# Kernel tuning notes

Hardware: AMD Instinct MI355X
Metric: run time of the kernel (lower is better)

Reference implementation:

```python
import jax, jax.numpy as jnp
import numpy as np

B, S, D, F, O = 4, 2048, 1024, 4096, 1024
E, NS, K = 4, 2, 2  # routed experts, shared experts, topk


def setup_inputs() -> dict:
    key = jax.random.key(0)
    ks = jax.random.split(key, 6)
    def w(k, shape, fan_in):
        return jax.random.normal(k, shape, jnp.float32) * (fan_in ** -0.5)
    return {
        "x": jax.random.normal(ks[0], (B, S, D), jnp.float32),
        "gate_w": w(ks[1], (D, E), D),
        "gate_b": jnp.zeros((E,), jnp.float32),
        "sw1": w(ks[2], (NS, D, F), D),  # shared experts, first linear
        "sb1": jnp.zeros((NS, F), jnp.float32),
        "sw2": w(ks[3], (NS, F, O), F),
        "sb2": jnp.zeros((NS, O), jnp.float32),
        "rw1": w(ks[4], (E, D, F), D),   # routed experts, first linear
        "rb1": jnp.zeros((E, F), jnp.float32),
        "rw2": w(ks[5], (E, F, O), F),
        "rb2": jnp.zeros((E, O), jnp.float32),
    }


def reference(x, gate_w, gate_b, sw1, sb1, sw2, sb2, rw1, rb1, rw2, rb2):
    # Gating (eval mode: no noise)
    weights = jax.nn.softmax(x @ gate_w + gate_b, axis=-1)      # [B,S,E]
    topk_w, topk_i = jax.lax.top_k(weights, K)                  # [B,S,K]

    # Shared experts: average of NS expert MLPs
    sh = jax.nn.relu(jnp.einsum('bsd,ndf->bsnf', x, sw1) + sb1)
    shared = (jnp.einsum('bsnf,nfo->bsno', sh, sw2) + sb2).sum(axis=2) / NS  # [B,S,O]

    # Routed experts: every expert applied densely, then one-hot-select topk.
    # Original computes expert(expanded_x) where expanded_x repeats x K times;
    # the result is identical per copy, so compute once per expert and gather.
    rh = jax.nn.relu(jnp.einsum('bsd,edf->bsef', x, rw1) + rb1)  # [B,S,E,F]
    eo = jnp.einsum('bsef,efo->bseo', rh, rw2) + rb2             # [B,S,E,O]
    gathered = jnp.take_along_axis(eo, topk_i[..., None], axis=2)  # [B,S,K,O]
    routed = (gathered * topk_w[..., None]).sum(axis=2)          # [B,S,O]

    return shared + routed
```

## Files before the change

kernel.cpp:

```cpp
#include <hip/hip_runtime.h>

typedef __bf16 bf16_t;
typedef __bf16 bf16x8 __attribute__((ext_vector_type(8)));
typedef float f32x4 __attribute__((ext_vector_type(4)));

constexpr int Tn = 4 * 2048;
constexpr int Dd = 1024;
constexpr int Ff = 4096;
constexpr int Oo = 1024;
constexpr int NEXP = 6;

__device__ __forceinline__ float ldin(const void* p, size_t i, int isf32) {
    return isf32 ? ((const float*)p)[i] : (float)((const bf16_t*)p)[i];
}

__global__ void detect_kernel(const unsigned int* __restrict__ xw, int* __restrict__ flag) {
    __shared__ int cnt;
    if (threadIdx.x == 0) cnt = 0;
    __syncthreads();
    int c = 0;
    for (int i = threadIdx.x; i < 16384; i += 256) {
        unsigned w = xw[i];
        if (((w >> 7) & 0xFFu) == 0xFFu) ++c;
    }
    atomicAdd(&cnt, c);
    __syncthreads();
    if (threadIdx.x == 0) flag[0] = (cnt >= 4) ? 1 : 0;
}

__global__ void cvt_x_kernel(const void* __restrict__ x, const int* __restrict__ flag,
                             bf16_t* __restrict__ xb) {
    int f = flag[0];
    size_t i = (size_t)blockIdx.x * 256 + threadIdx.x;
    xb[i] = (bf16_t)ldin(x, i, f);
}

__global__ void cvt_transpose_kernel(const void* __restrict__ src, size_t eofs,
                                     const int* __restrict__ flag,
                                     bf16_t* __restrict__ dst, int R, int C) {
    __shared__ bf16_t tile[32][33];
    int f = flag[0];
    int c0 = blockIdx.x * 32, r0 = blockIdx.y * 32;
    int tx = threadIdx.x, ty = threadIdx.y;
    #pragma unroll
    for (int i = 0; i < 32; i += 8)
        tile[ty + i][tx] = (bf16_t)ldin(src, eofs + (size_t)(r0 + ty + i) * C + c0 + tx, f);
    __syncthreads();
    #pragma unroll
    for (int i = 0; i < 32; i += 8)
        dst[(size_t)(c0 + ty + i) * R + r0 + tx] = tile[tx][ty + i];
}

__global__ void gate_kernel(const void* __restrict__ x, const void* __restrict__ gw,
                            const void* __restrict__ gb, const int* __restrict__ flag,
                            float* __restrict__ coef) {
    int f = flag[0];
    int t = blockIdx.x;
    int lane = threadIdx.x;
    float a0 = 0.f, a1 = 0.f, a2 = 0.f, a3 = 0.f;
    for (int d = lane; d < Dd; d += 64) {
        float xv = ldin(x, (size_t)t * Dd + d, f);
        a0 += xv * ldin(gw, (size_t)d * 4 + 0, f);
        a1 += xv * ldin(gw, (size_t)d * 4 + 1, f);
        a2 += xv * ldin(gw, (size_t)d * 4 + 2, f);
        a3 += xv * ldin(gw, (size_t)d * 4 + 3, f);
    }
    #pragma unroll
    for (int off = 32; off; off >>= 1) {
        a0 += __shfl_xor(a0, off);
        a1 += __shfl_xor(a1, off);
        a2 += __shfl_xor(a2, off);
        a3 += __shfl_xor(a3, off);
    }
    if (lane == 0) {
        float l[4] = {a0 + ldin(gb, 0, f), a1 + ldin(gb, 1, f),
                      a2 + ldin(gb, 2, f), a3 + ldin(gb, 3, f)};
        float mx = fmaxf(fmaxf(l[0], l[1]), fmaxf(l[2], l[3]));
        float e[4], s = 0.f;
        #pragma unroll
        for (int i = 0; i < 4; ++i) { e[i] = expf(l[i] - mx); s += e[i]; }
        float w[4];
        #pragma unroll
        for (int i = 0; i < 4; ++i) w[i] = e[i] / s;
        int i0 = 0;
        for (int i = 1; i < 4; ++i) if (w[i] > w[i0]) i0 = i;
        int i1 = -1;
        for (int i = 0; i < 4; ++i) { if (i == i0) continue; if (i1 < 0 || w[i] > w[i1]) i1 = i; }
        float c[8] = {0.5f, 0.5f, 0.f, 0.f, 0.f, 0.f, 0.f, 0.f};
        c[2 + i0] = w[i0];
        c[2 + i1] = w[i1];
        float* dst = coef + (size_t)t * 8;
        #pragma unroll
        for (int k = 0; k < 8; ++k) dst[k] = c[k];
    }
}

__global__ void init_acc_kernel(const float* __restrict__ coef, const void* __restrict__ sb2,
                                const void* __restrict__ rb2, const int* __restrict__ flag,
                                float* __restrict__ acc) {
    int f = flag[0];
    size_t idx = (size_t)blockIdx.x * 256 + threadIdx.x;
    int t = (int)(idx >> 10);
    int o = (int)(idx & 1023);
    const float* c = coef + (size_t)t * 8;
    float v = c[0] * ldin(sb2, o, f) + c[1] * ldin(sb2, Oo + o, f)
            + c[2] * ldin(rb2, o, f) + c[3] * ldin(rb2, Oo + o, f)
            + c[4] * ldin(rb2, 2 * Oo + o, f) + c[5] * ldin(rb2, 3 * Oo + o, f);
    acc[idx] = v;
}

__global__ void convert_kernel(const float* __restrict__ acc, const int* __restrict__ flag,
                               void* __restrict__ out) {
    int f = flag[0];
    size_t idx = (size_t)blockIdx.x * 256 + threadIdx.x;
    float v = acc[idx];
    if (v != v) v = 333.0f;
    if (f) ((float*)out)[idx] = v;
    else   ((bf16_t*)out)[idx] = (bf16_t)v;
}

template <int MODE>
__launch_bounds__(256, 2)
__global__ void gemm_kernel(const bf16_t* __restrict__ A, const bf16_t* __restrict__ Bt,
                            int M, int N, int K,
                            const void* __restrict__ bias, size_t b1_e,
                            const int* __restrict__ flag,
                            const float* __restrict__ coef,
                            bf16_t* __restrict__ obf, float* __restrict__ oacc) {
    constexpr int BM = 128, BN = 128, BK = 64;
    __shared__ __align__(16) bf16_t Al[BM * BK];
    __shared__ __align__(16) bf16_t Bl[BN * BK];

    const int tid = threadIdx.x;
    const int lane = tid & 63;
    const int wave = tid >> 6;
    const int wm = wave & 1, wn = wave >> 1;
    const int bm = blockIdx.x * BM;
    const int bn = blockIdx.y * BN;
    const int l15 = lane & 15;
    const int l4 = lane >> 4;
    const int r7 = l15 & 7;

    f32x4 acc[4][4] = {};

    for (int k0 = 0; k0 < K; k0 += BK) {
        #pragma unroll
        for (int it = 0; it < 4; ++it) {
            int q = it * 256 + tid;
            int row = q >> 3, c8s = q & 7;
            int k8 = c8s ^ (row & 7);
            const bf16_t* g = A + (size_t)(bm + row) * K + k0 + k8 * 8;
            __builtin_amdgcn_global_load_lds(
                (const __attribute__((address_space(1))) unsigned int*)g,
                (__attribute__((address_space(3))) unsigned int*)(&Al[q * 8]), 16, 0, 0);
        }
        #pragma unroll
        for (int it = 0; it < 4; ++it) {
            int q = it * 256 + tid;
            int row = q >> 3, c8s = q & 7;
            int k8 = c8s ^ (row & 7);
            const bf16_t* g = Bt + (size_t)(bn + row) * K + k0 + k8 * 8;
            __builtin_amdgcn_global_load_lds(
                (const __attribute__((address_space(1))) unsigned int*)g,
                (__attribute__((address_space(3))) unsigned int*)(&Bl[q * 8]), 16, 0, 0);
        }
        __syncthreads();
        #pragma unroll
        for (int kk = 0; kk < BK; kk += 32) {
            const int k8f = l4 + (kk >> 3);
            const int c8s = (k8f ^ r7) * 8;
            bf16x8 af[4], bfv[4];
            #pragma unroll
            for (int i = 0; i < 4; ++i)
                af[i] = *(const bf16x8*)&Al[(wm * 64 + i * 16 + l15) * BK + c8s];
            #pragma unroll
            for (int j = 0; j < 4; ++j)
                bfv[j] = *(const bf16x8*)&Bl[(wn * 64 + j * 16 + l15) * BK + c8s];
            #pragma unroll
            for (int i = 0; i < 4; ++i)
                #pragma unroll
                for (int j = 0; j < 4; ++j)
                    acc[i][j] = __builtin_amdgcn_mfma_f32_16x16x32_bf16(af[i], bfv[j], acc[i][j], 0, 0, 0);
        }
        __syncthreads();
    }

    if (MODE == 1) {
        int isf32 = flag[0];
        float bz[4];
        #pragma unroll
        for (int j = 0; j < 4; ++j)
            bz[j] = ldin(bias, b1_e + (size_t)(bn + wn * 64 + j * 16 + l15), isf32);
        #pragma unroll
        for (int i = 0; i < 4; ++i) {
            #pragma unroll
            for (int r = 0; r < 4; ++r) {
                int m = bm + wm * 64 + i * 16 + l4 * 4 + r;
                float cf = coef[(size_t)m * 8];
                #pragma unroll
                for (int j = 0; j < 4; ++j) {
                    float v = acc[i][j][r] + bz[j];
                    v = fmaxf(v, 0.f) * cf;
                    obf[(size_t)m * N + bn + wn * 64 + j * 16 + l15] = (bf16_t)v;
                }
            }
        }
    } else {
        #pragma unroll
        for (int i = 0; i < 4; ++i) {
            #pragma unroll
            for (int r = 0; r < 4; ++r) {
                int m = bm + wm * 64 + i * 16 + l4 * 4 + r;
                float* orow = oacc + (size_t)m * N + bn + wn * 64 + l15;
                #pragma unroll
                for (int j = 0; j < 4; ++j)
                    orow[j * 16] += acc[i][j][r];
            }
        }
    }
}

extern "C" void kernel_launch(void* const* d_in, const int* in_sizes, int n_in,
                              void* d_out, int out_size, void* d_ws, size_t ws_size,
                              hipStream_t stream) {
    const void* x      = d_in[0];
    const void* gate_w = d_in[1];
    const void* gate_b = d_in[2];
    const void* sw1    = d_in[3];
    const void* sb1    = d_in[4];
    const void* sw2    = d_in[5];
    const void* sb2    = d_in[6];
    const void* rw1    = d_in[7];
    const void* rb1    = d_in[8];
    const void* rw2    = d_in[9];
    const void* rb2    = d_in[10];

    char* ws = (char*)d_ws;
    int* flag = (int*)ws;
    size_t off = 256;
    bf16_t* W1T = (bf16_t*)(ws + off); off += (size_t)Ff * Dd * sizeof(bf16_t);
    bf16_t* W2T = (bf16_t*)(ws + off); off += (size_t)Oo * Ff * sizeof(bf16_t);
    bf16_t* xb  = (bf16_t*)(ws + off); off += (size_t)Tn * Dd * sizeof(bf16_t);
    float* coef = (float*)(ws + off);  off += (size_t)Tn * 8 * sizeof(float);
    float* accb = (float*)(ws + off);  off += (size_t)Tn * Oo * sizeof(float);
    bf16_t* Hs  = (bf16_t*)(ws + off);
    size_t rem = (ws_size > off) ? (ws_size - off) : 0;
    long tcap = (long)(rem / ((size_t)Ff * sizeof(bf16_t)));
    int Tc = (int)((tcap / 128) * 128);
    if (Tc < 128) Tc = 128;
    if (Tc > Tn) Tc = Tn;

    detect_kernel<<<1, 256, 0, stream>>>((const unsigned int*)x, flag);
    cvt_x_kernel<<<(Tn * Dd) / 256, 256, 0, stream>>>(x, flag, xb);
    gate_kernel<<<Tn, 64, 0, stream>>>(x, gate_w, gate_b, flag, coef);
    init_acc_kernel<<<(Tn * Oo) / 256, 256, 0, stream>>>(coef, sb2, rb2, flag, accb);

    dim3 tb(32, 8);
    for (int j = 0; j < NEXP; ++j) {
        const void* w1 = (j < 2) ? sw1 : rw1;
        const void* w2 = (j < 2) ? sw2 : rw2;
        const void* b1 = (j < 2) ? sb1 : rb1;
        int je = (j < 2) ? j : (j - 2);
        size_t w1_e = (size_t)je * Dd * Ff;
        size_t w2_e = (size_t)je * Ff * Oo;
        size_t b1_e = (size_t)je * Ff;

        cvt_transpose_kernel<<<dim3(Ff / 32, Dd / 32), tb, 0, stream>>>(w1, w1_e, flag, W1T, Dd, Ff);
        cvt_transpose_kernel<<<dim3(Oo / 32, Ff / 32), tb, 0, stream>>>(w2, w2_e, flag, W2T, Ff, Oo);

        for (int tok0 = 0; tok0 < Tn; tok0 += Tc) {
            int tc = (Tn - tok0 < Tc) ? (Tn - tok0) : Tc;
            gemm_kernel<1><<<dim3(tc / 128, Ff / 128), 256, 0, stream>>>(
                xb + (size_t)tok0 * Dd, W1T, tc, Ff, Dd,
                b1, b1_e, flag, coef + (size_t)tok0 * 8 + j, Hs, nullptr);
            gemm_kernel<2><<<dim3(tc / 128, Oo / 128), 256, 0, stream>>>(
                Hs, W2T, tc, Oo, Ff, nullptr, 0, flag, nullptr, nullptr, accb + (size_t)tok0 * Oo);
        }
    }

    convert_kernel<<<(Tn * Oo) / 256, 256, 0, stream>>>(accb, flag, d_out);
}
```

Measured before the change: 1.211 ms.

## Double-buffer GEMM LDS tiles with 256-row blocks, 8 waves and XCD-aware block remap

Reworks the bf16 MFMA GEMM to use 256x256 (first linear) and 256x128 (second linear) tiles with 512 threads. LDS is double-buffered so global-to-LDS loads for step t+2 overlap the MFMAs of step t, with hand-placed waitcnt and barriers. It also adds s_setprio around MFMA bursts and remaps block IDs so that blocks sharing tiles are grouped, aiming at better L2 locality across the XCDs. Larger tiles raise arithmetic intensity but increase register and LDS pressure, and they reduce the number of blocks available to fill the CUs.

Measured after the change: 1.402 ms. 15.8% more time.

```diff
diff --git a/kernel.cpp b/kernel.cpp
--- a/kernel.cpp
+++ b/kernel.cpp
@@ -119,101 +119,169 @@
     else   ((bf16_t*)out)[idx] = (bf16_t)v;
 }
 
-template <int MODE>
-__launch_bounds__(256, 2)
+template <int MODE, int BN_, int WM_>
+__launch_bounds__(512, 2)
 __global__ void gemm_kernel(const bf16_t* __restrict__ A, const bf16_t* __restrict__ Bt,
                             int M, int N, int K,
                             const void* __restrict__ bias, size_t b1_e,
                             const int* __restrict__ flag,
                             const float* __restrict__ coef,
                             bf16_t* __restrict__ obf, float* __restrict__ oacc) {
-    constexpr int BM = 128, BN = 128, BK = 64;
-    __shared__ __align__(16) bf16_t Al[BM * BK];
-    __shared__ __align__(16) bf16_t Bl[BN * BK];
+    constexpr int BM = 256, BK = 64;
+    constexpr int WN_ = 8 / WM_;
+    constexpr int NI = 16 / WM_;
+    constexpr int NJ = BN_ / (WN_ * 16);
+    constexpr int NIH = NI / 2;
+    constexpr int NJH = NJ / 2;
+    constexpr int ALOADS = 4;
+    constexpr int BLOADS = BN_ / 64;
+    constexpr int TOT = ALOADS + BLOADS;
+
+    __shared__ __align__(16) bf16_t Al[2][BM * BK];
+    __shared__ __align__(16) bf16_t Bl[2][BN_ * BK];
 
     const int tid = threadIdx.x;
     const int lane = tid & 63;
     const int wave = tid >> 6;
-    const int wm = wave & 1, wn = wave >> 1;
-    const int bm = blockIdx.x * BM;
-    const int bn = blockIdx.y * BN;
+    const int wm = wave / WN_;
+    const int wn = wave % WN_;
     const int l15 = lane & 15;
     const int l4 = lane >> 4;
     const int r7 = l15 & 7;
 
-    f32x4 acc[4][4] = {};
-
-    for (int k0 = 0; k0 < K; k0 += BK) {
-        #pragma unroll
-        for (int it = 0; it < 4; ++it) {
-            int q = it * 256 + tid;
-            int row = q >> 3, c8s = q & 7;
-            int k8 = c8s ^ (row & 7);
+    const int gx = gridDim.x;
+    const int nwg = gx * gridDim.y;
+    const int id = blockIdx.y * gx + blockIdx.x;
+    const int cpx = nwg >> 3;
+    const int sid = (id & 7) * cpx + (id >> 3);
+    const int bm = (sid % gx) * BM;
+    const int bn = (sid / gx) * BN_;
+
+    const int nK = K / BK;
+
+    auto stage = [&](int t, int b) {
+        const int k0 = t * BK;
+        #pragma unroll
+        for (int it = 0; it < ALOADS; ++it) {
+            int q = it * 512 + tid;
+            int row = q >> 3, c8 = q & 7;
+            int k8 = c8 ^ (row & 7);
             const bf16_t* g = A + (size_t)(bm + row) * K + k0 + k8 * 8;
             __builtin_amdgcn_global_load_lds(
                 (const __attribute__((address_space(1))) unsigned int*)g,
-                (__attribute__((address_space(3))) unsigned int*)(&Al[q * 8]), 16, 0, 0);
-        }
-        #pragma unroll
-        for (int it = 0; it < 4; ++it) {
-            int q = it * 256 + tid;
-            int row = q >> 3, c8s = q & 7;
-            int k8 = c8s ^ (row & 7);
+                (__attribute__((address_space(3))) unsigned int*)(&Al[b][q * 8]), 16, 0, 0);
+        }
+        #pragma unroll
+        for (int it = 0; it < BLOADS; ++it) {
+            int q = it * 512 + tid;
+            int row = q >> 3, c8 = q & 7;
+            int k8 = c8 ^ (row & 7);
             const bf16_t* g = Bt + (size_t)(bn + row) * K + k0 + k8 * 8;
             __builtin_amdgcn_global_load_lds(
                 (const __attribute__((address_space(1))) unsigned int*)g,
-                (__attribute__((address_space(3))) unsigned int*)(&Bl[q * 8]), 16, 0, 0);
-        }
-        __syncthreads();
-        #pragma unroll
-        for (int kk = 0; kk < BK; kk += 32) {
-            const int k8f = l4 + (kk >> 3);
-            const int c8s = (k8f ^ r7) * 8;
-            bf16x8 af[4], bfv[4];
+                (__attribute__((address_space(3))) unsigned int*)(&Bl[b][q * 8]), 16, 0, 0);
+        }
+    };
+
+    f32x4 acc[NI][NJ] = {};
+
+    stage(0, 0);
+    if (nK > 1) {
+        stage(1, 1);
+        if constexpr (TOT == 8) asm volatile("s_waitcnt vmcnt(8)" ::: "memory");
+        else                    asm volatile("s_waitcnt vmcnt(6)" ::: "memory");
+    } else {
+        asm volatile("s_waitcnt vmcnt(0)" ::: "memory");
+    }
+    __builtin_amdgcn_sched_barrier(0);
+    __builtin_amdgcn_s_barrier();
+    __builtin_amdgcn_sched_barrier(0);
+
+    const int a_off0 = ((l4 + 0) ^ r7) * 8;
+    const int a_off1 = ((l4 + 4) ^ r7) * 8;
+    const int arow = wm * (NI * 16) + l15;
+    const int brow = wn * (NJ * 16) + l15;
+
+    for (int t = 0; t < nK; ++t) {
+        const bf16_t* __restrict__ Ab = Al[t & 1];
+        const bf16_t* __restrict__ Bb = Bl[t & 1];
+        bf16x8 bfv[NJ][2];
+        bf16x8 af[NIH][2];
+        #pragma unroll
+        for (int j = 0; j < NJ; ++j) {
+            bfv[j][0] = *(const bf16x8*)&Bb[(brow + j * 16) * BK + a_off0];
+            bfv[j][1] = *(const bf16x8*)&Bb[(brow + j * 16) * BK + a_off1];
+        }
+        #pragma unroll
+        for (int ih = 0; ih < 2; ++ih) {
             #pragma unroll
-            for (int i = 0; i < 4; ++i)
-                af[i] = *(const bf16x8*)&Al[(wm * 64 + i * 16 + l15) * BK + c8s];
+            for (int i = 0; i < NIH; ++i) {
+                af[i][0] = *(const bf16x8*)&Ab[(arow + (ih * NIH + i) * 16) * BK + a_off0];
+                af[i][1] = *(const bf16x8*)&Ab[(arow + (ih * NIH + i) * 16) * BK + a_off1];
+            }
             #pragma unroll
-            for (int j = 0; j < 4; ++j)
-                bfv[j] = *(const bf16x8*)&Bl[(wn * 64 + j * 16 + l15) * BK + c8s];
-            #pragma unroll
-            for (int i = 0; i < 4; ++i)
+            for (int jh = 0; jh < 2; ++jh) {
+                __builtin_amdgcn_s_setprio(1);
                 #pragma unroll
-                for (int j = 0; j < 4; ++j)
-                    acc[i][j] = __builtin_amdgcn_mfma_f32_16x16x32_bf16(af[i], bfv[j], acc[i][j], 0, 0, 0);
-        }
-        __syncthreads();
+                for (int kx = 0; kx < 2; ++kx)
+                    #pragma unroll
+                    for (int i = 0; i < NIH; ++i)
+                        #pragma unroll
+                        for (int j = 0; j < NJH; ++j)
+                            acc[ih * NIH + i][jh * NJH + j] =
+                                __builtin_amdgcn_mfma_f32_16x16x32_bf16(
+                                    af[i][kx], bfv[jh * NJH + j][kx],
+                                    acc[ih * NIH + i][jh * NJH + j], 0, 0, 0);
+                __builtin_amdgcn_s_setprio(0);
+            }
+        }
+        if (t + 1 < nK) {
+            asm volatile("s_waitcnt lgkmcnt(0)" ::: "memory");
+            __builtin_amdgcn_sched_barrier(0);
+            __builtin_amdgcn_s_barrier();
+            __builtin_amdgcn_sched_barrier(0);
+            if (t + 2 < nK) {
+                stage(t + 2, t & 1);
+                if constexpr (TOT == 8) asm volatile("s_waitcnt vmcnt(8)" ::: "memory");
+                else                    asm volatile("s_waitcnt vmcnt(6)" ::: "memory");
+            } else {
+                asm volatile("s_waitcnt vmcnt(0)" ::: "memory");
+            }
+            __builtin_amdgcn_sched_barrier(0);
+            __builtin_amdgcn_s_barrier();
+            __builtin_amdgcn_sched_barrier(0);
+        }
     }
 
     if (MODE == 1) {
-        int isf32 = flag[0];
-        float bz[4];
-        #pragma unroll
-        for (int j = 0; j < 4; ++j)
-            bz[j] = ldin(bias, b1_e + (size_t)(bn + wn * 64 + j * 16 + l15), isf32);
-        #pragma unroll
-        for (int i = 0; i < 4; ++i) {
+        const int isf32 = flag[0];
+        float bz[NJ];
+        #pragma unroll
+        for (int j = 0; j < NJ; ++j)
+            bz[j] = ldin(bias, b1_e + (size_t)(bn + wn * (NJ * 16) + j * 16 + l15), isf32);
+        #pragma unroll
+        for (int i = 0; i < NI; ++i) {
             #pragma unroll
             for (int r = 0; r < 4; ++r) {
-                int m = bm + wm * 64 + i * 16 + l4 * 4 + r;
+                int m = bm + wm * (NI * 16) + i * 16 + l4 * 4 + r;
                 float cf = coef[(size_t)m * 8];
                 #pragma unroll
-                for (int j = 0; j < 4; ++j) {
+                for (int j = 0; j < NJ; ++j) {
                     float v = acc[i][j][r] + bz[j];
                     v = fmaxf(v, 0.f) * cf;
-                    obf[(size_t)m * N + bn + wn * 64 + j * 16 + l15] = (bf16_t)v;
+                    obf[(size_t)m * N + bn + wn * (NJ * 16) + j * 16 + l15] = (bf16_t)v;
                 }
             }
         }
     } else {
         #pragma unroll
-        for (int i = 0; i < 4; ++i) {
+        for (int i = 0; i < NI; ++i) {
             #pragma unroll
             for (int r = 0; r < 4; ++r) {
-                int m = bm + wm * 64 + i * 16 + l4 * 4 + r;
-                float* orow = oacc + (size_t)m * N + bn + wn * 64 + l15;
+                int m = bm + wm * (NI * 16) + i * 16 + l4 * 4 + r;
+                float* orow = oacc + (size_t)m * N + bn + wn * (NJ * 16) + l15;
                 #pragma unroll
-                for (int j = 0; j < 4; ++j)
+                for (int j = 0; j < NJ; ++j)
                     orow[j * 16] += acc[i][j][r];
             }
         }
@@ -246,8 +314,8 @@
     bf16_t* Hs  = (bf16_t*)(ws + off);
     size_t rem = (ws_size > off) ? (ws_size - off) : 0;
     long tcap = (long)(rem / ((size_t)Ff * sizeof(bf16_t)));
-    int Tc = (int)((tcap / 128) * 128);
-    if (Tc < 128) Tc = 128;
+    int Tc = (int)((tcap / 256) * 256);
+    if (Tc < 256) Tc = 256;
     if (Tc > Tn) Tc = Tn;
 
     detect_kernel<<<1, 256, 0, stream>>>((const unsigned int*)x, flag);
@@ -270,11 +338,12 @@
 
         for (int tok0 = 0; tok0 < Tn; tok0 += Tc) {
             int tc = (Tn - tok0 < Tc) ? (Tn - tok0) : Tc;
-            gemm_kernel<1><<<dim3(tc / 128, Ff / 128), 256, 0, stream>>>(
+            gemm_kernel<1, 256, 2><<<dim3(tc / 256, Ff / 256), 512, 0, stream>>>(
                 xb + (size_t)tok0 * Dd, W1T, tc, Ff, Dd,
                 b1, b1_e, flag, coef + (size_t)tok0 * 8 + j, Hs, nullptr);
-            gemm_kernel<2><<<dim3(tc / 128, Oo / 128), 256, 0, stream>>>(
-                Hs, W2T, tc, Oo, Ff, nullptr, 0, flag, nullptr, nullptr, accb + (size_t)tok0 * Oo);
+            gemm_kernel<2, 128, 4><<<dim3(tc / 256, Oo / 128), 512, 0, stream>>>(
+                Hs, W2T, tc, Oo, Ff, nullptr, 0, flag, nullptr, nullptr,
+                accb + (size_t)tok0 * Oo);
         }
     }
 
```

## Gather routed tokens per expert and run routed GEMMs only on selected rows

Applied to the files above, without the earlier changes.

The gate kernel now builds a per-expert token list with atomics. A finalize kernel pads each list to 128 rows, pointing padded entries at a dummy token whose coefficient is zero. Routed-expert GEMMs gather A rows through that list and scatter-accumulate outputs by token index. Blocks beyond the expert's padded count exit early, so each routed expert processes only about half the tokens instead of all of them. In exchange this adds atomics, indirect loads and scattered stores, and the dummy row reads past the end of xb.

Result: slower. 1.303 ms (+7.6%).

```diff
diff --git a/kernel.cpp b/kernel.cpp
--- a/kernel.cpp
+++ b/kernel.cpp
@@ -8,7 +8,6 @@
 constexpr int Dd = 1024;
 constexpr int Ff = 4096;
 constexpr int Oo = 1024;
-constexpr int NEXP = 6;
 
 __device__ __forceinline__ float ldin(const void* p, size_t i, int isf32) {
     return isf32 ? ((const float*)p)[i] : (float)((const bf16_t*)p)[i];
@@ -26,6 +25,10 @@
     atomicAdd(&cnt, c);
     __syncthreads();
     if (threadIdx.x == 0) flag[0] = (cnt >= 4) ? 1 : 0;
+}
+
+__global__ void zero_cnt_kernel(int* __restrict__ cnt) {
+    if (threadIdx.x < 4) cnt[threadIdx.x] = 0;
 }
 
 __global__ void cvt_x_kernel(const void* __restrict__ x, const int* __restrict__ flag,
@@ -53,7 +56,8 @@
 
 __global__ void gate_kernel(const void* __restrict__ x, const void* __restrict__ gw,
                             const void* __restrict__ gb, const int* __restrict__ flag,
-                            float* __restrict__ coef) {
+                            float* __restrict__ coef, int* __restrict__ cnt,
+                            int* __restrict__ tlist) {
     int f = flag[0];
     int t = blockIdx.x;
     int lane = threadIdx.x;
@@ -92,7 +96,24 @@
         float* dst = coef + (size_t)t * 8;
         #pragma unroll
         for (int k = 0; k < 8; ++k) dst[k] = c[k];
-    }
+        int p0 = atomicAdd(&cnt[i0], 1);
+        tlist[(size_t)i0 * Tn + p0] = t;
+        int p1 = atomicAdd(&cnt[i1], 1);
+        tlist[(size_t)i1 * Tn + p1] = t;
+    }
+}
+
+__global__ void finalize_route_kernel(const int* __restrict__ cnt, int* __restrict__ cntp,
+                                      int* __restrict__ tlist, float* __restrict__ coef) {
+    int lane = threadIdx.x;
+    #pragma unroll
+    for (int e = 0; e < 4; ++e) {
+        int c = cnt[e]; if (c > Tn) c = Tn;
+        int p = (c + 127) & ~127;
+        if (lane == 0) cntp[e] = p;
+        for (int i = c + lane; i < p; i += 64) tlist[(size_t)e * Tn + i] = Tn;
+    }
+    if (lane < 8) coef[(size_t)Tn * 8 + lane] = 0.f;
 }
 
 __global__ void init_acc_kernel(const float* __restrict__ coef, const void* __restrict__ sb2,
@@ -126,8 +147,16 @@
                             const void* __restrict__ bias, size_t b1_e,
                             const int* __restrict__ flag,
                             const float* __restrict__ coef,
-                            bf16_t* __restrict__ obf, float* __restrict__ oacc) {
+                            bf16_t* __restrict__ obf, float* __restrict__ oacc,
+                            const int* __restrict__ tl, const int* __restrict__ cntp,
+                            int tok0, int joff) {
     constexpr int BM = 128, BN = 128, BK = 64;
+
+    if constexpr (MODE >= 3) {
+        int rem = cntp[0] - tok0;
+        if ((int)blockIdx.x * BM >= rem) return;
+    }
+
     __shared__ __align__(16) bf16_t Al[BM * BK];
     __shared__ __align__(16) bf16_t Bl[BN * BK];
 
@@ -141,6 +170,12 @@
     const int l4 = lane >> 4;
     const int r7 = l15 & 7;
 
+    int ar[4];
+    if constexpr (MODE == 3) {
+        #pragma unroll
+        for (int it = 0; it < 4; ++it) ar[it] = tl[bm + (tid >> 3) + it * 32];
+    }
+
     f32x4 acc[4][4] = {};
 
     for (int k0 = 0; k0 < K; k0 += BK) {
@@ -149,7 +184,11 @@
             int q = it * 256 + tid;
             int row = q >> 3, c8s = q & 7;
             int k8 = c8s ^ (row & 7);
-            const bf16_t* g = A + (size_t)(bm + row) * K + k0 + k8 * 8;
+            const bf16_t* g;
+            if constexpr (MODE == 3)
+                g = A + (size_t)ar[it] * K + k0 + k8 * 8;
+            else
+                g = A + (size_t)(bm + row) * K + k0 + k8 * 8;
             __builtin_amdgcn_global_load_lds(
                 (const __attribute__((address_space(1))) unsigned int*)g,
                 (__attribute__((address_space(3))) unsigned int*)(&Al[q * 8]), 16, 0, 0);
@@ -185,7 +224,7 @@
         __syncthreads();
     }
 
-    if (MODE == 1) {
+    if constexpr (MODE == 1 || MODE == 3) {
         int isf32 = flag[0];
         float bz[4];
         #pragma unroll
@@ -196,7 +235,13 @@
             #pragma unroll
             for (int r = 0; r < 4; ++r) {
                 int m = bm + wm * 64 + i * 16 + l4 * 4 + r;
-                float cf = coef[(size_t)m * 8];
+                float cf;
+                if constexpr (MODE == 3) {
+                    int token = tl[m];
+                    cf = coef[(size_t)token * 8 + joff];
+                } else {
+                    cf = coef[(size_t)m * 8];
+                }
                 #pragma unroll
                 for (int j = 0; j < 4; ++j) {
                     float v = acc[i][j][r] + bz[j];
@@ -211,7 +256,13 @@
             #pragma unroll
             for (int r = 0; r < 4; ++r) {
                 int m = bm + wm * 64 + i * 16 + l4 * 4 + r;
-                float* orow = oacc + (size_t)m * N + bn + wn * 64 + l15;
+                float* orow;
+                if constexpr (MODE == 4) {
+                    int token = tl[m];
+                    orow = oacc + (size_t)token * N + bn + wn * 64 + l15;
+                } else {
+                    orow = oacc + (size_t)m * N + bn + wn * 64 + l15;
+                }
                 #pragma unroll
                 for (int j = 0; j < 4; ++j)
                     orow[j * 16] += acc[i][j][r];
@@ -241,8 +292,14 @@
     bf16_t* W1T = (bf16_t*)(ws + off); off += (size_t)Ff * Dd * sizeof(bf16_t);
     bf16_t* W2T = (bf16_t*)(ws + off); off += (size_t)Oo * Ff * sizeof(bf16_t);
     bf16_t* xb  = (bf16_t*)(ws + off); off += (size_t)Tn * Dd * sizeof(bf16_t);
-    float* coef = (float*)(ws + off);  off += (size_t)Tn * 8 * sizeof(float);
-    float* accb = (float*)(ws + off);  off += (size_t)Tn * Oo * sizeof(float);
+    float* coef = (float*)(ws + off);  off += (size_t)(Tn + 1) * 8 * sizeof(float);
+    off = (off + 255) & ~(size_t)255;
+    int* cnt    = (int*)(ws + off);    off += 256;
+    int* cntp   = (int*)(ws + off);    off += 256;
+    int* tlist  = (int*)(ws + off);    off += (size_t)4 * Tn * sizeof(int);
+    off = (off + 255) & ~(size_t)255;
+    float* accb = (float*)(ws + off);  off += (size_t)(Tn + 1) * Oo * sizeof(float);
+    off = (off + 255) & ~(size_t)255;
     bf16_t* Hs  = (bf16_t*)(ws + off);
     size_t rem = (ws_size > off) ? (ws_size - off) : 0;
     long tcap = (long)(rem / ((size_t)Ff * sizeof(bf16_t)));
@@ -251,30 +308,47 @@
     if (Tc > Tn) Tc = Tn;
 
     detect_kernel<<<1, 256, 0, stream>>>((const unsigned int*)x, flag);
+    zero_cnt_kernel<<<1, 64, 0, stream>>>(cnt);
     cvt_x_kernel<<<(Tn * Dd) / 256, 256, 0, stream>>>(x, flag, xb);
-    gate_kernel<<<Tn, 64, 0, stream>>>(x, gate_w, gate_b, flag, coef);
+    gate_kernel<<<Tn, 64, 0, stream>>>(x, gate_w, gate_b, flag, coef, cnt, tlist);
+    finalize_route_kernel<<<1, 64, 0, stream>>>(cnt, cntp, tlist, coef);
     init_acc_kernel<<<(Tn * Oo) / 256, 256, 0, stream>>>(coef, sb2, rb2, flag, accb);
 
     dim3 tb(32, 8);
-    for (int j = 0; j < NEXP; ++j) {
-        const void* w1 = (j < 2) ? sw1 : rw1;
-        const void* w2 = (j < 2) ? sw2 : rw2;
-        const void* b1 = (j < 2) ? sb1 : rb1;
-        int je = (j < 2) ? j : (j - 2);
-        size_t w1_e = (size_t)je * Dd * Ff;
-        size_t w2_e = (size_t)je * Ff * Oo;
-        size_t b1_e = (size_t)je * Ff;
-
-        cvt_transpose_kernel<<<dim3(Ff / 32, Dd / 32), tb, 0, stream>>>(w1, w1_e, flag, W1T, Dd, Ff);
-        cvt_transpose_kernel<<<dim3(Oo / 32, Ff / 32), tb, 0, stream>>>(w2, w2_e, flag, W2T, Ff, Oo);
-
+
+    for (int j = 0; j < 2; ++j) {
+        size_t w1_e = (size_t)j * Dd * Ff;
+        size_t w2_e = (size_t)j * Ff * Oo;
+        size_t b1_e = (size_t)j * Ff;
+        cvt_transpose_kernel<<<dim3(Ff / 32, Dd / 32), tb, 0, stream>>>(sw1, w1_e, flag, W1T, Dd, Ff);
+        cvt_transpose_kernel<<<dim3(Oo / 32, Ff / 32), tb, 0, stream>>>(sw2, w2_e, flag, W2T, Ff, Oo);
         for (int tok0 = 0; tok0 < Tn; tok0 += Tc) {
             int tc = (Tn - tok0 < Tc) ? (Tn - tok0) : Tc;
             gemm_kernel<1><<<dim3(tc / 128, Ff / 128), 256, 0, stream>>>(
                 xb + (size_t)tok0 * Dd, W1T, tc, Ff, Dd,
-                b1, b1_e, flag, coef + (size_t)tok0 * 8 + j, Hs, nullptr);
+                sb1, b1_e, flag, coef + (size_t)tok0 * 8 + j, Hs, nullptr,
+                nullptr, nullptr, 0, 0);
             gemm_kernel<2><<<dim3(tc / 128, Oo / 128), 256, 0, stream>>>(
-                Hs, W2T, tc, Oo, Ff, nullptr, 0, flag, nullptr, nullptr, accb + (size_t)tok0 * Oo);
+                Hs, W2T, tc, Oo, Ff, nullptr, 0, flag, nullptr, nullptr,
+                accb + (size_t)tok0 * Oo, nullptr, nullptr, 0, 0);
+        }
+    }
+
+    for (int e = 0; e < 4; ++e) {
+        size_t w1_e = (size_t)e * Dd * Ff;
+        size_t w2_e = (size_t)e * Ff * Oo;
+        size_t b1_e = (size_t)e * Ff;
+        cvt_transpose_kernel<<<dim3(Ff / 32, Dd / 32), tb, 0, stream>>>(rw1, w1_e, flag, W1T, Dd, Ff);
+        cvt_transpose_kernel<<<dim3(Oo / 32, Ff / 32), tb, 0, stream>>>(rw2, w2_e, flag, W2T, Ff, Oo);
+        for (int tok0 = 0; tok0 < Tn; tok0 += Tc) {
+            int tc = (Tn - tok0 < Tc) ? (Tn - tok0) : Tc;
+            gemm_kernel<3><<<dim3(tc / 128, Ff / 128), 256, 0, stream>>>(
+                xb, W1T, tc, Ff, Dd,
+                rb1, b1_e, flag, coef, Hs, nullptr,
+                tlist + (size_t)e * Tn + tok0, cntp + e, tok0, 2 + e);
+            gemm_kernel<4><<<dim3(tc / 128, Oo / 128), 256, 0, stream>>>(
+                Hs, W2T, tc, Oo, Ff, nullptr, 0, flag, nullptr, nullptr,
+                accb, tlist + (size_t)e * Tn + tok0, cntp + e, tok0, 0);
         }
     }
 
```
